# Kernel tuning notes

Measured on AMD Instinct MI355X. Metric: run time of the kernel, lower is better.

Reference implementation:

```python
import jax, jax.numpy as jnp
import numpy as np

N, M, KNN, KUP, POS_DIM = 15872, 35637, 5, 20, 32


def _pos_emb_table(n, d):
    # transformer-style sinusoidal table (matches PosEmb._define_pos_emb)
    pos = np.arange(n, dtype=np.float32)[:, None]
    i2 = np.arange(0, d, 2, dtype=np.float32)
    div = 10000.0 ** (i2 / d)
    pe = np.zeros((n, d), dtype=np.float32)
    pe[:, 0::2] = np.sin(pos / div)
    pe[:, 1::2] = np.cos(pos / div)
    return jnp.asarray(pe)


def _lrelu(x):
    return jnp.where(x > 0, x, 0.2 * x)


def _gather(x, idx):
    # x: [B,n,d], idx: [B,m,k] -> [B,m,k,d]
    return jax.vmap(lambda xb, ib: xb[ib])(x, idx)


def _knn_idx(x, k):
    # x: [B,n,d]; k nearest excluding self (torch knn drops column 0 of topk)
    xx = jnp.sum(x * x, axis=-1)
    neg = 2.0 * jnp.einsum('bnd,bmd->bnm', x, x) - xx[:, :, None] - xx[:, None, :]
    _, idx = jax.lax.top_k(neg, k + 1)
    return idx[..., 1:]


def _emb_block(feat, idx, ec_w1, ec_s1, ec_h1, ec_w2, ec_b2,
               w1, s1, h1, w2, s2, h2, w3, s3, h3, w4, b4):
    # get_graph_feature: [B,n,k,2*in] = cat(nbr - ctr, ctr)
    nbr = _gather(feat, idx)
    ctr = jnp.broadcast_to(feat[:, :, None, :], nbr.shape)
    e = jnp.concatenate([nbr - ctr, ctr], axis=-1)
    # edge_conv (1x1 conv2d = per-edge linear); BN folded into scale/shift (eval mode)
    e = _lrelu(jnp.einsum('bnkc,oc->bnko', e, ec_w1) * ec_s1 + ec_h1)
    e = jnp.einsum('bnkc,oc->bnko', e, ec_w2) + ec_b2
    f1 = jnp.max(e, axis=2)                                   # max over k neighbors -> [B,n,out]
    fmax = jnp.broadcast_to(jnp.max(f1, axis=1, keepdims=True), f1.shape)
    favg = jnp.broadcast_to(jnp.mean(f1, axis=1, keepdims=True), f1.shape)
    h = jnp.concatenate([feat, f1, fmax, favg], axis=-1)      # [B,n,3*out+in]
    # fc_out: 1x1 conv1d stack = per-point MLP with folded BN + LeakyReLU
    h = _lrelu(h @ w1.T * s1 + h1)
    h = _lrelu(h @ w2.T * s2 + h2)
    h = _lrelu(h @ w3.T * s3 + h3)
    return h @ w4.T + b4


def _forward(lx, ldx, pos_emb,
             b0_ec_w1, b0_ec_s1, b0_ec_h1, b0_ec_w2, b0_ec_b2,
             b0_fc_w1, b0_fc_s1, b0_fc_h1, b0_fc_w2, b0_fc_s2, b0_fc_h2,
             b0_fc_w3, b0_fc_s3, b0_fc_h3, b0_fc_w4, b0_fc_b4,
             b1_ec_w1, b1_ec_s1, b1_ec_h1, b1_ec_w2, b1_ec_b2,
             b1_fc_w1, b1_fc_s1, b1_fc_h1, b1_fc_w2, b1_fc_s2, b1_fc_h2,
             b1_fc_w3, b1_fc_s3, b1_fc_h3, b1_fc_w4, b1_fc_b4,
             up_inputs, up_w0, up_s0, up_h0, up_w_rest, up_s_rest, up_h_rest, up_wf, up_bf,
             dec_w0, dec_b0, dec_w1, dec_b1, dec_w2, dec_b2, dec_w3, dec_b3,
             dec_w4, dec_b4, dec_wf, dec_bf,
             idx0, up_idx):
    B = ldx.shape[0]
    feat_in = jnp.concatenate([ldx, jnp.broadcast_to(pos_emb[None], (B,) + pos_emb.shape)], axis=-1)  # [B,N,35]
    f0 = _emb_block(feat_in, idx0,
                    b0_ec_w1, b0_ec_s1, b0_ec_h1, b0_ec_w2, b0_ec_b2,
                    b0_fc_w1, b0_fc_s1, b0_fc_h1, b0_fc_w2, b0_fc_s2, b0_fc_h2,
                    b0_fc_w3, b0_fc_s3, b0_fc_h3, b0_fc_w4, b0_fc_b4)   # [B,N,64]
    idx1 = _knn_idx(f0, KNN)                                            # dynamic feature-space KNN
    f1 = _emb_block(f0, idx1,
                    b1_ec_w1, b1_ec_s1, b1_ec_h1, b1_ec_w2, b1_ec_b2,
                    b1_fc_w1, b1_fc_s1, b1_fc_h1, b1_fc_w2, b1_fc_s2, b1_fc_h2,
                    b1_fc_w3, b1_fc_s3, b1_fc_h3, b1_fc_w4, b1_fc_b4)   # [B,N,128]
    x_feat = jnp.concatenate([feat_in, f0, f1], axis=-1)                # [B,N,227]
    # Upscale: SIREN-activated 1x1-conv stack -> softmax interpolation weights over KUP lo-res nbrs
    h = jnp.sin(jnp.einsum('bmkc,oc->bmko', up_inputs[:B], up_w0) * up_s0 + up_h0)
    for i in range(up_w_rest.shape[0]):
        h = jnp.sin(jnp.einsum('bmkc,oc->bmko', h, up_w_rest[i]) * up_s_rest[i] + up_h_rest[i])
    logits = jnp.einsum('bmkc,oc->bmko', h, up_wf) + up_bf              # [B,M,KUP,1]
    w = jax.nn.softmax(logits, axis=2)
    grouped = _gather(x_feat, up_idx)                                   # [B,M,KUP,227]
    z = jnp.sum(w * grouped, axis=2)                                    # [B,M,227]
    # SIREN decoder: dims [227,256,128,64,32,16,3]; zip with 5 mods applies first 5 layers + head
    h = jnp.sin(30.0 * (z @ dec_w0.T + dec_b0))
    h = jnp.sin(h @ dec_w1.T + dec_b1)
    h = jnp.sin(h @ dec_w2.T + dec_b2)
    h = jnp.sin(h @ dec_w3.T + dec_b3)
    h = jnp.sin(h @ dec_w4.T + dec_b4)
    return h @ dec_wf.T + dec_bf                                        # [B,M,3]


def setup_inputs():
    key = jax.random.key(0)
    ks = iter(jax.random.split(key, 100))
    def rn(*s):
        return jax.random.normal(next(ks), s, jnp.float32) * 0.05
    def sc(*s):
        return jax.random.uniform(next(ks), s, jnp.float32, minval=0.5, maxval=1.5)
    inp = {}
    inp['lx'] = jax.random.normal(next(ks), (1, N, 3), jnp.float32)
    inp['ldx'] = jax.random.normal(next(ks), (1, N, 3), jnp.float32)
    inp['pos_emb'] = _pos_emb_table(N, POS_DIM)
    inp['idx0'] = jax.random.randint(next(ks), (1, N, KNN), 0, N - 1)
    # EmbModule 0: in=35, out=64
    inp['b0_ec_w1'], inp['b0_ec_s1'], inp['b0_ec_h1'] = rn(128, 70), sc(128), rn(128)
    inp['b0_ec_w2'], inp['b0_ec_b2'] = rn(64, 128), rn(64)
    inp['b0_fc_w1'], inp['b0_fc_s1'], inp['b0_fc_h1'] = rn(192, 227), sc(192), rn(192)
    inp['b0_fc_w2'], inp['b0_fc_s2'], inp['b0_fc_h2'] = rn(128, 192), sc(128), rn(128)
    inp['b0_fc_w3'], inp['b0_fc_s3'], inp['b0_fc_h3'] = rn(64, 128), sc(64), rn(64)
    inp['b0_fc_w4'], inp['b0_fc_b4'] = rn(64, 64), rn(64)
    # EmbModule 1: in=64, out=128
    inp['b1_ec_w1'], inp['b1_ec_s1'], inp['b1_ec_h1'] = rn(256, 128), sc(256), rn(256)
    inp['b1_ec_w2'], inp['b1_ec_b2'] = rn(128, 256), rn(128)
    inp['b1_fc_w1'], inp['b1_fc_s1'], inp['b1_fc_h1'] = rn(384, 448), sc(384), rn(384)
    inp['b1_fc_w2'], inp['b1_fc_s2'], inp['b1_fc_h2'] = rn(256, 384), sc(256), rn(256)
    inp['b1_fc_w3'], inp['b1_fc_s3'], inp['b1_fc_h3'] = rn(128, 256), sc(128), rn(128)
    inp['b1_fc_w4'], inp['b1_fc_b4'] = rn(128, 128), rn(128)
    inp['up_inputs'] = jax.random.uniform(next(ks), (1, M, KUP, 7), jnp.float32)
    inp['up_idx'] = jax.random.randint(next(ks), (1, M, KUP), 0, N - 1)
    inp['up_w0'], inp['up_s0'], inp['up_h0'] = rn(128, 7), sc(128), rn(128)
    inp['up_w_rest'], inp['up_s_rest'], inp['up_h_rest'] = rn(7, 128, 128), sc(7, 128), rn(7, 128)
    inp['up_wf'], inp['up_bf'] = rn(1, 128), rn(1)
    # SIREN decoder
    dd = [227, 256, 128, 64, 32, 16]
    for i in range(5):
        inp['dec_w%d' % i], inp['dec_b%d' % i] = rn(dd[i + 1], dd[i]), rn(dd[i + 1])
    inp['dec_wf'], inp['dec_bf'] = rn(3, 16), rn(3)
    return inp


def reference(lx, ldx, pos_emb, idx0,
              b0_ec_w1, b0_ec_s1, b0_ec_h1, b0_ec_w2, b0_ec_b2,
              b0_fc_w1, b0_fc_s1, b0_fc_h1, b0_fc_w2, b0_fc_s2, b0_fc_h2,
              b0_fc_w3, b0_fc_s3, b0_fc_h3, b0_fc_w4, b0_fc_b4,
              b1_ec_w1, b1_ec_s1, b1_ec_h1, b1_ec_w2, b1_ec_b2,
              b1_fc_w1, b1_fc_s1, b1_fc_h1, b1_fc_w2, b1_fc_s2, b1_fc_h2,
              b1_fc_w3, b1_fc_s3, b1_fc_h3, b1_fc_w4, b1_fc_b4,
              up_inputs, up_idx, up_w0, up_s0, up_h0,
              up_w_rest, up_s_rest, up_h_rest, up_wf, up_bf,
              dec_w0, dec_b0, dec_w1, dec_b1, dec_w2, dec_b2, dec_w3, dec_b3,
              dec_w4, dec_b4, dec_wf, dec_bf):
    return _forward(lx, ldx, pos_emb,
                    b0_ec_w1, b0_ec_s1, b0_ec_h1, b0_ec_w2, b0_ec_b2,
                    b0_fc_w1, b0_fc_s1, b0_fc_h1, b0_fc_w2, b0_fc_s2, b0_fc_h2,
                    b0_fc_w3, b0_fc_s3, b0_fc_h3, b0_fc_w4, b0_fc_b4,
                    b1_ec_w1, b1_ec_s1, b1_ec_h1, b1_ec_w2, b1_ec_b2,
                    b1_fc_w1, b1_fc_s1, b1_fc_h1, b1_fc_w2, b1_fc_s2, b1_fc_h2,
                    b1_fc_w3, b1_fc_s3, b1_fc_h3, b1_fc_w4, b1_fc_b4,
                    up_inputs, up_w0, up_s0, up_h0, up_w_rest, up_s_rest, up_h_rest, up_wf, up_bf,
                    dec_w0, dec_b0, dec_w1, dec_b1, dec_w2, dec_b2, dec_w3, dec_b3,
                    dec_w4, dec_b4, dec_wf, dec_bf,
                    idx0, up_idx)
```

## Files before the change

### kernel.cpp

```cpp
#include <hip/hip_runtime.h>
#include <hip/hip_bf16.h>
#include <math.h>

#define N_PTS 15872
#define M_PTS 35637
#define KNN_K 5
#define KUP   20
#define UP_ROWS (M_PTS * KUP)
#define NTILE (N_PTS/32)
#define N_EDGE (N_PTS*KNN_K)
#define CDIV(a,b) (((a)+(b)-1)/(b))

typedef __hip_bfloat16 bf16;
typedef unsigned int uint;
typedef unsigned short ushort_t;
__device__ __forceinline__ float b2f(bf16 x){ return __bfloat162float(x); }

__device__ __forceinline__ uint f2bf_bits(float x){
  uint u = __float_as_uint(x);
  return (u + 0x7FFFu + ((u>>16)&1u)) >> 16;
}

__device__ __forceinline__ ushort_t f2h_bits(float x){
  union { _Float16 h; ushort_t u; } c; c.h = (_Float16)x; return c.u;
}

typedef __attribute__((ext_vector_type(8))) short bf16x8;
typedef __attribute__((ext_vector_type(8))) _Float16 f16x8;
typedef __attribute__((ext_vector_type(2))) __fp16 fp16x2_t;
typedef __attribute__((ext_vector_type(16))) float f32x16;
union FragAB { bf16x8 v; uint u[4]; };
union FragB  { bf16x8 v; uint4 q; };
union FragH  { f16x8 v; uint4 q; _Float16 h[8]; };
union Acc16  { f32x16 v; float f[16]; };
union H2U    { fp16x2_t h; uint u; };

__global__ void flag_k(const uint* __restrict__ pos_raw, int* __restrict__ flag){
  if (threadIdx.x == 0 && blockIdx.x == 0)
    flag[0] = (pos_raw[0] == 0x3F800000u) ? 1 : 0;
}

struct CvtTab { const void* src[52]; int start[52]; };
__global__ __launch_bounds__(256) void cvt_all_k(CvtTab tab, float* __restrict__ dst,
                                                 const int* __restrict__ flag, int total){
  int i = blockIdx.x*256 + threadIdx.x;
  if (i >= total) return;
  int s = 0;
#pragma unroll 1
  for (int k = 1; k < 52; k++) if (tab.start[k] <= i) s = k;
  int off = i - tab.start[s];
  float v = flag[0] ? b2f(((const bf16*)tab.src[s])[off]) : ((const float*)tab.src[s])[off];
  dst[i] = v;
}

__global__ void packfrag16_k(const float* __restrict__ w, const float* __restrict__ sr,
                             ushort_t* __restrict__ out, int n){
  int i = blockIdx.x*256 + threadIdx.x;
  if (i >= n) return;
  int j = i & 7;
  int lam = (i >> 3) & 63;
  int fg = i >> 9;
  int t = fg & 3, ks = (fg >> 2) & 1, Q = (fg >> 3) & 3, l = fg >> 5;
  int nn = t*32 + (lam & 31);
  int kk = Q*32 + ks*16 + ((j>>2)<<3) + ((lam>>5)<<2) + (j&3);
  float x = w[l*16384 + nn*128 + kk] * sr[l*128 + nn];
  out[i] = f2h_bits(x);
}

struct PackTab { const float* src[18]; int N[18], K[18], ldk[18], Kpad[18], start[18]; };
__global__ __launch_bounds__(256) void packw_all_k(PackTab t, ushort_t* __restrict__ whi,
                                                   ushort_t* __restrict__ wlo, int total){
  int i = blockIdx.x*256 + threadIdx.x;
  if (i >= total) return;
  int s = 0;
#pragma unroll 1
  for (int q = 1; q < 18; q++) if (t.start[q] <= i) s = q;
  int ii = i - t.start[s];
  int j = ii & 7;
  int lane = (ii >> 3) & 63;
  int fr = ii >> 9;
  int nq = t.Kpad[s] >> 5;
  int ks = fr & 1;
  int q  = (fr >> 1) % nq;
  int nt = (fr >> 1) / nq;
  int n = nt*32 + (lane & 31);
  int k = q*32 + ks*16 + (lane >> 5)*8 + j;
  float x = (n < t.N[s] && k < t.K[s]) ? t.src[s][(size_t)n*t.ldk[s] + k] : 0.f;
  uint hb = f2bf_bits(x);
  uint lb = f2bf_bits(x - __uint_as_float(hb << 16));
  whi[i] = (ushort_t)hb;
  wlo[i] = (ushort_t)lb;
}

__global__ void packknn_k(const float* __restrict__ xf, const float* __restrict__ nr,
                          ushort_t* __restrict__ ahi, ushort_t* __restrict__ alo,
                          ushort_t* __restrict__ bhi, ushort_t* __restrict__ blo){
  int i = blockIdx.x*256 + threadIdx.x;
  if (i >= NTILE*5*64*8) return;
  int e = i & 7;
  int lane = (i >> 3) & 63;
  int rest = i >> 9;
  int kc = rest % 5, jt = rest / 5;
  int n = jt*32 + (lane & 31);
  int k = kc*16 + (lane >> 5)*8 + e;
  float f = (k < 64) ? xf[(size_t)n*227 + 35 + k] : 0.f;
  float av, bv;
  if (k < 64)      { av = 2.f*f;   bv = f; }
  else if (k == 64){ av = nr[n];   bv = -1.f; }
  else if (k == 65){ av = 1.f;     bv = -nr[n]; }
  else             { av = 0.f;     bv = 0.f; }
  uint ah = f2bf_bits(av); uint al = f2bf_bits(av - __uint_as_float(ah<<16));
  uint bh = f2bf_bits(bv); uint bl = f2bf_bits(bv - __uint_as_float(bh<<16));
  ahi[i] = (ushort_t)ah; alo[i] = (ushort_t)al;
  bhi[i] = (ushort_t)bh; blo[i] = (ushort_t)bl;
}

__global__ void fillmark_k(bf16* __restrict__ out, int n){
  int i = blockIdx.x*256 + threadIdx.x;
  if (i < n) out[i] = __float2bfloat16(12345.0f);
}

template<int ACT>
__global__ __launch_bounds__(256) void gemm_mfma_k(
    const float* __restrict__ A, int lda, int K, int M,
    const ushort_t* __restrict__ wh, const ushort_t* __restrict__ wl,
    int woff, int KqTot,
    const float* __restrict__ scale, const float* __restrict__ shift,
    float* __restrict__ C, int ldc, int N)
{
  __shared__ __align__(16) uint slab[64*128];
  const int tid = threadIdx.x;
  const int lane = tid & 63;
  const int wv = tid >> 6;
  const int np = lane & 31;
  const int hb2 = lane >> 5;
  const int rhalf = wv & 1, thalf = wv >> 1;
  const int rb = blockIdx.x * 64;
  const int tbase = blockIdx.y * 4;
  const int row_l = rhalf*32 + np;
  int NtLoc = (N >> 5) - tbase; if (NtLoc > 4) NtLoc = 4;

  Acc16 acc[2];
#pragma unroll
  for (int u=0;u<2;u++)
#pragma unroll
    for (int i=0;i<16;i++) acc[u].f[i] = 0.f;

#pragma unroll 1
  for (int k0 = 0; k0 < K; k0 += 128) {
    for (int e = tid; e < 64*32; e += 256) {
      int r = e >> 5, g = e & 31;
      int gr = rb + r;
      uint p[4];
#pragma unroll
      for (int u=0;u<4;u++){
        int k = k0 + g*4 + u;
        float f = (gr < M && k < K) ? A[(size_t)gr*lda + k] : 0.f;
        uint hb = f2bf_bits(f);
        uint lb = f2bf_bits(f - __uint_as_float(hb<<16));
        p[u] = (hb<<16) | lb;
      }
      *(uint4*)&slab[r*128 + (((g ^ r) & 31)<<2)] = make_uint4(p[0],p[1],p[2],p[3]);
    }
    __syncthreads();
    int qb = k0 >> 5;
    int KqLoc = KqTot - qb; if (KqLoc > 4) KqLoc = 4;
#pragma unroll 1
    for (int q = 0; q < KqLoc; q++){
#pragma unroll
      for (int ks = 0; ks < 2; ks++){
        int g0 = q*8 + ks*4 + hb2*2;
        uint4 a0 = *(const uint4*)&slab[row_l*128 + ((((g0  ) ^ row_l) & 31)<<2)];
        uint4 a1 = *(const uint4*)&slab[row_l*128 + ((((g0+1) ^ row_l) & 31)<<2)];
        uint au[8] = {a0.x,a0.y,a0.z,a0.w,a1.x,a1.y,a1.z,a1.w};
        FragAB ah, al;
#pragma unroll
        for (int p=0;p<4;p++){
          ah.u[p] = (au[2*p]>>16)     | (au[2*p+1] & 0xFFFF0000u);
          al.u[p] = (au[2*p]&0xFFFFu) | (au[2*p+1]<<16);
        }
#pragma unroll
        for (int u=0;u<2;u++){
          int t = thalf + u*2;
          if (t < NtLoc){
            size_t fb = (size_t)woff + ((size_t)(((tbase+t)*KqTot + qb + q)*2 + ks))*512 + (size_t)lane*8;
            FragB bh, bl;
            bh.q = *(const uint4*)(wh + fb);
            bl.q = *(const uint4*)(wl + fb);
            acc[u].v = __builtin_amdgcn_mfma_f32_32x32x16_bf16(ah.v, bh.v, acc[u].v, 0,0,0);
            acc[u].v = __builtin_amdgcn_mfma_f32_32x32x16_bf16(al.v, bh.v, acc[u].v, 0,0,0);
            acc[u].v = __builtin_amdgcn_mfma_f32_32x32x16_bf16(ah.v, bl.v, acc[u].v, 0,0,0);
          }
        }
      }
    }
    __syncthreads();
  }

#pragma unroll
  for (int u=0;u<2;u++){
    int t = thalf + u*2;
    if (t < NtLoc){
      int col = (tbase+t)*32 + np;
      float scv = scale[col], shv = shift[col];
#pragma unroll
      for (int reg=0;reg<16;reg++){
        int r32 = (reg&3) + 8*(reg>>2) + 4*hb2;
        int gr = rb + rhalf*32 + r32;
        if (gr < M){
          float v = acc[u].f[reg]*scv + shv;
          if (ACT==1) v = v > 0.f ? v : 0.2f*v;
          C[(size_t)gr*ldc + col] = v;
        }
      }
    }
  }
}

struct MLayer { int K, N, Kq, Nt, woff, soff, hoff, epi, act; float gmul; };
struct MCfg { MLayer L[6]; };

template<int NL, int OUTMODE>
__global__ __launch_bounds__(256) void mlp_fused_k(
    const float* __restrict__ A0, int lda0, int K0, int M,
    MCfg cfg,
    const ushort_t* __restrict__ wh, const ushort_t* __restrict__ wl,
    const float* __restrict__ wc,
    float* __restrict__ Cout, int ldc,
    void* __restrict__ oflg, const int* __restrict__ flag)
{
  __shared__ __align__(16) uint slab[64*256];
  const int tid = threadIdx.x;
  const int lane = tid & 63;
  const int wv = tid >> 6;
  const int np = lane & 31;
  const int hb2 = lane >> 5;
  const int rhalf = wv & 1, thalf = wv >> 1;
  const int rb = blockIdx.x * 64;
  const int row_l = rhalf*32 + np;

  for (int e = tid; e < 64*64; e += 256) {
    int r = e >> 6, g = e & 63;
    int gr = rb + r;
    uint p[4];
#pragma unroll
    for (int u=0;u<4;u++){
      int k = g*4+u;
      float f = (gr < M && k < K0) ? A0[(size_t)gr*lda0 + k] : 0.f;
      uint hb = f2bf_bits(f);
      uint lb = f2bf_bits(f - __uint_as_float(hb<<16));
      p[u] = (hb<<16) | lb;
    }
    *(uint4*)&slab[r*256 + (((g ^ r) & 63)<<2)] = make_uint4(p[0],p[1],p[2],p[3]);
  }
  __syncthreads();

#pragma unroll 1
  for (int l = 0; l < NL; l++){
    const int N = cfg.L[l].N, Kq = cfg.L[l].Kq, Nt = cfg.L[l].Nt;
    const int woff = cfg.L[l].woff, soff = cfg.L[l].soff, hoff = cfg.L[l].hoff;
    const int epi = cfg.L[l].epi, actf = cfg.L[l].act;
    const float gmul = cfg.L[l].gmul;
    Acc16 acc[4];
#pragma unroll
    for (int u=0;u<4;u++)
#pragma unroll
      for (int i=0;i<16;i++) acc[u].f[i] = 0.f;

#pragma unroll 1
    for (int q = 0; q < Kq; q++){
#pragma unroll
      for (int ks = 0; ks < 2; ks++){
        int g0 = (q*32 + ks*16 + hb2*8) >> 2;
        uint4 a0 = *(const uint4*)&slab[row_l*256 + ((((g0  ) ^ row_l) & 63)<<2)];
        uint4 a1 = *(const uint4*)&slab[row_l*256 + ((((g0+1) ^ row_l) & 63)<<2)];
        uint au[8] = {a0.x,a0.y,a0.z,a0.w,a1.x,a1.y,a1.z,a1.w};
        FragAB ah, al;
#pragma unroll
        for (int p=0;p<4;p++){
          ah.u[p] = (au[2*p]>>16)     | (au[2*p+1] & 0xFFFF0000u);
          al.u[p] = (au[2*p]&0xFFFFu) | (au[2*p+1]<<16);
        }
#pragma unroll
        for (int u=0;u<4;u++){
          int t = thalf + u*2;
          if (t < Nt){
            size_t fb = (size_t)woff + ((size_t)((t*Kq + q)*2 + ks))*512 + (size_t)lane*8;
            FragB bh, bl;
            bh.q = *(const uint4*)(wh + fb);
            bl.q = *(const uint4*)(wl + fb);
            acc[u].v = __builtin_amdgcn_mfma_f32_32x32x16_bf16(ah.v, bh.v, acc[u].v, 0,0,0);
            acc[u].v = __builtin_amdgcn_mfma_f32_32x32x16_bf16(al.v, bh.v, acc[u].v, 0,0,0);
            acc[u].v = __builtin_amdgcn_mfma_f32_32x32x16_bf16(ah.v, bl.v, acc[u].v, 0,0,0);
          }
        }
      }
    }
    __syncthreads();
#pragma unroll
    for (int u=0;u<4;u++){
      int t = thalf + u*2;
      if (t < Nt){
        int col = t*32 + np;
        if (col < N){
          float scv = (epi==0) ? wc[soff+col] : 0.f;
          float shv = wc[hoff+col];
#pragma unroll
          for (int reg=0;reg<16;reg++){
            int r32 = (reg&3) + 8*(reg>>2) + 4*hb2;
            float v = acc[u].f[reg];
            if (epi==0)      v = v*scv + shv;
            else if (epi==1) v = v + shv;
            else             v = (v + shv)*gmul;
            if (actf==1)      v = v > 0.f ? v : 0.2f*v;
            else if (actf==2) v = __sinf(v);
            if (l == NL-1){
              int gr = rb + rhalf*32 + r32;
              if (gr < M){
                if (OUTMODE==0) Cout[(size_t)gr*ldc + col] = v;
                else {
                  if (!(fabsf(v) < 1e30f)) v = 777.0f;
                  size_t oi = (size_t)gr*3 + col;
                  if (flag[0]) ((bf16*)oflg)[oi] = __float2bfloat16(v);
                  else         ((float*)oflg)[oi] = v;
                }
              }
            } else {
              int r = rhalf*32 + r32;
              uint hb = f2bf_bits(v);
              uint lb = f2bf_bits(v - __uint_as_float(hb<<16));
              slab[r*256 + ((((col>>2) ^ r) & 63)<<2) + (col&3)] = (hb<<16) | lb;
            }
          }
        }
      }
    }
    __syncthreads();
  }
}

#define INS5(tv, tj, v, j) \
  if ((v) > tv[4]){ tv[4]=(v); tj[4]=(j); \
    _Pragma("unroll") \
    for (int q=4;q>0;q--) \
      if (tv[q] > tv[q-1]){ float tf=tv[q-1]; tv[q-1]=tv[q]; tv[q]=tf; \
                            int ti=tj[q-1]; tj[q-1]=tj[q]; tj[q]=ti; } }

__global__ __launch_bounds__(256) void knn_mfma_k(
    const ushort_t* __restrict__ ahi, const ushort_t* __restrict__ alo,
    const ushort_t* __restrict__ bhi, const ushort_t* __restrict__ blo,
    int* __restrict__ out)
{
  __shared__ float mv[4][32][5];
  __shared__ int   mjj[4][32][5];
  const int tid = threadIdx.x;
  const int lane = tid & 63;
  const int wv = tid >> 6;
  const int np = lane & 31;
  const int hb2 = lane >> 5;
  const int it = blockIdx.x;
  const int ig = it*32 + np;

  FragB vh[5], vl[5];
  {
    size_t bb = (size_t)(it*5)*512 + (size_t)lane*8;
#pragma unroll
    for (int kc=0;kc<5;kc++){
      vh[kc].q = *(const uint4*)(bhi + bb + kc*512);
      vl[kc].q = *(const uint4*)(blo + bb + kc*512);
    }
  }

  float tv[5] = {-1e30f,-1e30f,-1e30f,-1e30f,-1e30f};
  int   tj[5] = {0,0,0,0,0};

  FragB uh[5], ul[5], nh[5], nl[5];
  {
    size_t ab = (size_t)(wv*5)*512 + (size_t)lane*8;
#pragma unroll
    for (int kc=0;kc<5;kc++){
      uh[kc].q = *(const uint4*)(ahi + ab + kc*512);
      ul[kc].q = *(const uint4*)(alo + ab + kc*512);
    }
  }

#pragma unroll 1
  for (int t = 0; t < NTILE/4; t++){
    int jt = wv + t*4;
    if (t+1 < NTILE/4){
      size_t an = (size_t)((jt+4)*5)*512 + (size_t)lane*8;
#pragma unroll
      for (int kc=0;kc<5;kc++){
        nh[kc].q = *(const uint4*)(ahi + an + kc*512);
        nl[kc].q = *(const uint4*)(alo + an + kc*512);
      }
    }
    Acc16 acc;
#pragma unroll
    for (int q=0;q<16;q++) acc.f[q] = 0.f;
#pragma unroll
    for (int kc=0;kc<5;kc++){
      acc.v = __builtin_amdgcn_mfma_f32_32x32x16_bf16(uh[kc].v, vh[kc].v, acc.v, 0,0,0);
      acc.v = __builtin_amdgcn_mfma_f32_32x32x16_bf16(ul[kc].v, vh[kc].v, acc.v, 0,0,0);
      acc.v = __builtin_amdgcn_mfma_f32_32x32x16_bf16(uh[kc].v, vl[kc].v, acc.v, 0,0,0);
    }
    int jb = jt*32 + 4*hb2;
#pragma unroll
    for (int reg=0;reg<16;reg++){
      int j = jb + (reg&3) + 8*(reg>>2);
      float v = acc.f[reg];
      if (j != ig) { INS5(tv, tj, v, j); }
    }
    if (t+1 < NTILE/4){
#pragma unroll
      for (int kc=0;kc<5;kc++){ uh[kc] = nh[kc]; ul[kc] = nl[kc]; }
    }
  }

#pragma unroll
  for (int s=0;s<5;s++){
    float ov = __shfl_xor(tv[s], 32, 64);
    int   oj = __shfl_xor(tj[s], 32, 64);
    INS5(tv, tj, ov, oj);
  }
  if (hb2 == 0){
#pragma unroll
    for (int s=0;s<5;s++){ mv[wv][np][s] = tv[s]; mjj[wv][np][s] = tj[s]; }
  }
  __syncthreads();
  if (tid < 32){
    float bv[5]; int bj[5];
#pragma unroll
    for (int s=0;s<5;s++){ bv[s] = mv[0][tid][s]; bj[s] = mjj[0][tid][s]; }
#pragma unroll
    for (int w=1;w<4;w++)
#pragma unroll
      for (int s=0;s<5;s++){
        float v = mv[w][tid][s]; int j = mjj[w][tid][s];
        INS5(bv, bj, v, j);
      }
    int gi = it*32 + tid;
#pragma unroll
    for (int s=0;s<5;s++) out[gi*KNN_K + s] = bj[s];
  }
}

__global__ __launch_bounds__(256) void siren_fused_k(
    const void* __restrict__ upin,
    const ushort_t* __restrict__ wf16,
    const float* __restrict__ W0c, const float* __restrict__ S0c, const float* __restrict__ H0c,
    const float* __restrict__ HRc,
    const float* __restrict__ WFc, const float* __restrict__ BFc,
    float* __restrict__ logits, const int* __restrict__ flag)
{
  __shared__ float intile[4*32*8];
  __shared__ __align__(16) float w0s[128*8];
  __shared__ __align__(16) float hrs[7*128];
  __shared__ __align__(16) float wfs[128];
  __shared__ float bfs[1];

  const int tid  = threadIdx.x;
  const int lane = tid & 63;
  const int wv   = tid >> 6;
  const int np   = lane & 31;
  const int hb2  = lane >> 5;
  const int rowbase = blockIdx.x * 128 + wv * 32;
  const int isbf = flag[0];
  float* intw = intile + wv*32*8;

  for (int e = tid; e < 128*7; e += 256){
    int c = e/7, k = e%7;
    w0s[c*8+k] = W0c[e]*S0c[c];
  }
  if (tid < 128) w0s[tid*8+7] = H0c[tid];
  for (int e = tid; e < 7*128; e += 256) hrs[e] = HRc[e];
  if (tid < 128) wfs[tid] = WFc[tid];
  if (tid == 0) bfs[0] = BFc[0];
  for (int e = lane; e < 32*7; e += 64) {
    int r = e/7, k = e%7;
    int gr = rowbase + r;
    float v = 0.f;
    if (gr < UP_ROWS)
      v = isbf ? b2f(((const bf16*)upin)[(size_t)gr*7+k]) : ((const float*)upin)[(size_t)gr*7+k];
    intw[r*8+k] = v;
  }
  __syncthreads();

  uint st0[16], st1[16];
  {
    float xin[7];
#pragma unroll
    for (int k=0;k<7;k++) xin[k] = intw[np*8+k];
#pragma unroll
    for (int g = 0; g < 16; g++){
      float xs[4];
#pragma unroll
      for (int j = 0; j < 4; j++){
        int c = g*8 + hb2*4 + j;
        const float4 wa = *(const float4*)&w0s[c*8];
        const float4 wb = *(const float4*)&w0s[c*8+4];
        float a = wb.w;
        a += xin[0]*wa.x; a += xin[1]*wa.y; a += xin[2]*wa.z; a += xin[3]*wa.w;
        a += xin[4]*wb.x; a += xin[5]*wb.y; a += xin[6]*wb.z;
        xs[j] = __sinf(a);
      }
      H2U u0,u1;
      u0.h = __builtin_amdgcn_cvt_pkrtz(xs[0],xs[1]);
      u1.h = __builtin_amdgcn_cvt_pkrtz(xs[2],xs[3]);
      st0[g] = u0.u; st1[g] = u1.u;
    }
  }

  FragH fr[8];
#pragma unroll
  for (int m = 0; m < 8; m++)
    fr[m].q = make_uint4(st0[2*m], st1[2*m], st0[2*m+1], st1[2*m+1]);

  uint nst0[16], nst1[16];
#pragma unroll 1
  for (int l = 0; l < 7; l++) {
#pragma unroll
    for (int tp = 0; tp < 2; tp++){
      Acc16 acc0, acc1;
#pragma unroll
      for (int i=0;i<16;i++){ acc0.f[i] = 0.f; acc1.f[i] = 0.f; }
#pragma unroll
      for (int m = 0; m < 8; m++){
        int fb = (((l*8 + m)*4 + tp*2) << 9) + lane*8;
        FragH bh0, bh1;
        bh0.q = *(const uint4*)(wf16 + fb);
        bh1.q = *(const uint4*)(wf16 + fb + 512);
        acc0.v = __builtin_amdgcn_mfma_f32_32x32x16_f16(bh0.v, fr[m].v, acc0.v, 0,0,0);
        acc1.v = __builtin_amdgcn_mfma_f32_32x32x16_f16(bh1.v, fr[m].v, acc1.v, 0,0,0);
      }
#pragma unroll
      for (int rg = 0; rg < 4; rg++){
        int g0 = (tp*2+0)*4 + rg;
        const float4 b0v = *(const float4*)&hrs[l*128 + g0*8 + hb2*4];
        float x0 = __sinf(acc0.f[rg*4+0] + b0v.x);
        float x1 = __sinf(acc0.f[rg*4+1] + b0v.y);
        float x2 = __sinf(acc0.f[rg*4+2] + b0v.z);
        float x3 = __sinf(acc0.f[rg*4+3] + b0v.w);
        H2U u0,u1;
        u0.h = __builtin_amdgcn_cvt_pkrtz(x0,x1);
        u1.h = __builtin_amdgcn_cvt_pkrtz(x2,x3);
        nst0[g0] = u0.u; nst1[g0] = u1.u;

        int g1 = (tp*2+1)*4 + rg;
        const float4 b1v = *(const float4*)&hrs[l*128 + g1*8 + hb2*4];
        float y0 = __sinf(acc1.f[rg*4+0] + b1v.x);
        float y1 = __sinf(acc1.f[rg*4+1] + b1v.y);
        float y2 = __sinf(acc1.f[rg*4+2] + b1v.z);
        float y3 = __sinf(acc1.f[rg*4+3] + b1v.w);
        H2U v0,v1;
        v0.h = __builtin_amdgcn_cvt_pkrtz(y0,y1);
        v1.h = __builtin_amdgcn_cvt_pkrtz(y2,y3);
        nst0[g1] = v0.u; nst1[g1] = v1.u;
      }
    }
    if (l < 6){
#pragma unroll
      for (int m = 0; m < 8; m++)
        fr[m].q = make_uint4(nst0[2*m], nst1[2*m], nst0[2*m+1], nst1[2*m+1]);
    }
  }

  {
    float a = 0.f;
#pragma unroll
    for (int g = 0; g < 16; g++){
      const float4 w4 = *(const float4*)&wfs[g*8 + hb2*4];
      H2U u0,u1; u0.u = nst0[g]; u1.u = nst1[g];
      a += (float)u0.h.x*w4.x + (float)u0.h.y*w4.y
         + (float)u1.h.x*w4.z + (float)u1.h.y*w4.w;
    }
    a += __shfl_xor(a, 32, 64);
    int gr = rowbase + np;
    if (hb2 == 0 && gr < UP_ROWS) logits[gr] = a + bfs[0];
  }
}

__global__ void featin_k(const void* __restrict__ ldx, const void* __restrict__ pos,
                         float* __restrict__ xf, const int* __restrict__ flag){
  int i = blockIdx.x*256 + threadIdx.x;
  if (i >= N_PTS*35) return;
  int n = i / 35, c = i % 35;
  float v;
  if (flag[0]) {
    v = (c < 3) ? b2f(((const bf16*)ldx)[n*3+c]) : b2f(((const bf16*)pos)[n*32 + (c-3)]);
  } else {
    v = (c < 3) ? ((const float*)ldx)[n*3+c] : ((const float*)pos)[n*32 + (c-3)];
  }
  xf[(size_t)n*227 + c] = v;
}

__global__ void gather_e_k(const float* __restrict__ xf, int coff, int CIN,
                           const int* __restrict__ idx, float* __restrict__ e,
                           int n0, int np){
  int W2 = 2*CIN;
  int i = blockIdx.x*256 + threadIdx.x;
  if (i >= np*KNN_K*W2) return;
  int c = i % W2; int ek = i / W2;
  int nl = ek / KNN_K, k = ek % KNN_K;
  int n = n0 + nl;
  int j = idx[n*KNN_K + k];
  float out;
  if (c < CIN) out = xf[(size_t)j*227 + coff + c] - xf[(size_t)n*227 + coff + c];
  else         out = xf[(size_t)n*227 + coff + (c-CIN)];
  e[(size_t)ek*W2 + c] = out;
}

__global__ void kmax_k(const float* __restrict__ e2, int C, int ld, float* __restrict__ f1,
                       int n0, int np){
  int i = blockIdx.x*256 + threadIdx.x;
  if (i >= np*C) return;
  int nl = i / C, c = i % C;
  float v = -1e30f;
  for (int k=0;k<KNN_K;k++) v = fmaxf(v, e2[((size_t)nl*KNN_K+k)*ld + c]);
  f1[(size_t)(n0+nl)*C + c] = v;
}

template<int C>
__global__ __launch_bounds__(256) void reduce1_k(const float* __restrict__ X, int n,
                                                 float* __restrict__ pmax, float* __restrict__ psum){
  const int tid = threadIdx.x;
  const int c = tid % C;
  const int r0 = tid / C;
  const int TPR = 256 / C;
  float vmax = -1e30f, vsum = 0.f;
  for (int row = blockIdx.x * TPR + r0; row < n; row += gridDim.x * TPR) {
    float v = X[(size_t)row * C + c];
    vmax = fmaxf(vmax, v); vsum += v;
  }
  __shared__ float smax[256], ssum[256];
  smax[tid]=vmax; ssum[tid]=vsum;
  __syncthreads();
  if (tid < C) {
    for (int q=1;q<TPR;q++){ vmax=fmaxf(vmax, smax[q*C+c]); vsum += ssum[q*C+c]; }
    pmax[blockIdx.x*C + c] = vmax; psum[blockIdx.x*C + c] = vsum;
  }
}

template<int C>
__global__ __launch_bounds__(256) void red2fold_k(
    const float* __restrict__ pmax, const float* __restrict__ psum,
    int nblk, float invn,
    const float* __restrict__ W, int ldw, int off1, int off2,
    const float* __restrict__ scale, const float* __restrict__ shift,
    float* __restrict__ out, int N)
{
  __shared__ float smax[C], ssum[C];
  int tid = threadIdx.x;
  if (tid < C){
    float vmax=-1e30f, vsum=0.f;
    for (int b=0;b<nblk;b++){ vmax=fmaxf(vmax,pmax[b*C+tid]); vsum+=psum[b*C+tid]; }
    smax[tid]=vmax; ssum[tid]=vsum*invn;
  }
  __syncthreads();
  for (int n = tid; n < N; n += 256){
    const float* wr = W + (size_t)n*ldw;
    float s = 0.f;
    for (int j=0;j<C;j++) s += wr[off1+j]*smax[j];
    for (int j=0;j<C;j++) s += wr[off2+j]*ssum[j];
    out[n] = s*scale[n] + shift[n];
  }
}

__global__ void concat2_k(const float* __restrict__ xf, int coff, int CF,
                          const float* __restrict__ f1, int C,
                          float* __restrict__ h, int n0, int np){
  int W = CF + C;
  int i = blockIdx.x*256 + threadIdx.x;
  if (i >= np*W) return;
  int nl = i / W, c = i % W;
  int n = n0 + nl;
  float v = (c < CF) ? xf[(size_t)n*227 + coff + c] : f1[(size_t)n*C + (c-CF)];
  h[(size_t)nl*W + c] = v;
}

__global__ void norms_k(const float* __restrict__ xf, float* __restrict__ nr){
  int n = blockIdx.x*256 + threadIdx.x;
  if (n >= N_PTS) return;
  const float* p = xf + (size_t)n*227 + 35;
  float s = 0.f;
  for (int d=0;d<64;d++) s += p[d]*p[d];
  nr[n] = s;
}

__global__ __launch_bounds__(256) void softgather_k(const float* __restrict__ logits,
                                                    const int* __restrict__ up_idx,
                                                    const float* __restrict__ xf,
                                                    float* __restrict__ z){
  __shared__ float lw[4][KUP]; __shared__ int li[4][KUP];
  int sub = threadIdx.x >> 6;
  int tid = threadIdx.x & 63;
  int m = blockIdx.x*4 + sub;
  bool ok = (m < M_PTS);
  if (ok && tid < KUP){
    lw[sub][tid] = logits[(size_t)m*KUP + tid];
    li[sub][tid] = up_idx[(size_t)m*KUP + tid];
  }
  __syncthreads();
  if (ok){
    float mx = -1e30f;
    for (int k=0;k<KUP;k++) mx = fmaxf(mx, lw[sub][k]);
    float w[KUP]; float s = 0.f;
    for (int k=0;k<KUP;k++){ w[k] = expf(lw[sub][k]-mx); s += w[k]; }
    float inv = 1.f/s;
    for (int c = tid; c < 227; c += 64){
      float acc = 0.f;
      for (int k=0;k<KUP;k++) acc += w[k] * xf[(size_t)li[sub][k]*227 + c];
      z[(size_t)m*227 + c] = acc*inv;
    }
  }
}

extern "C" void kernel_launch(void* const* d_in, const int* in_sizes, int n_in,
                              void* d_out, int out_size, void* d_ws, size_t ws_size,
                              hipStream_t stream) {
  const int *idx0  = (const int*)d_in[3];
  const int *upidx = (const int*)d_in[37];

  float* ws = (float*)d_ws;
  float* x_feat = ws;
  float* f1b    = ws + 3602944;
  float* pmax   = ws + 5634560;
  float* psum   = ws + 5667328;
  float* fold0  = pmax + 24576;
  float* fold1  = psum + 24576;
  int*   flag   = (int*)(ws + 5700352);
  int*   idx1   = (int*)(ws + 5700368);
  float* nrm    = ws + 5779728;
  float* logits = ws + 5795600;
  float* wcvt   = ws + 6508352;
  float* S      = ws + 7214400;
  ushort_t* whi  = (ushort_t*)(S + 9662464);
  ushort_t* wlo  = whi + 114688;
  ushort_t* gwhi = wlo + 114688;
  ushort_t* gwlo = gwhi + 503808;

  const size_t NEED = (size_t)(7214400 + 9662464) * 4
                    + (size_t)(114688*2 + 503808*2) * 2;
  if (ws_size < NEED) {
    fillmark_k<<<CDIV(out_size,256),256,0,stream>>>((bf16*)d_out, out_size);
    return;
  }

  flag_k<<<1,64,0,stream>>>((const uint*)d_in[2], flag);
  CvtTab tab;
  int wcoff = 0, seg = 0;
  auto CVT = [&](int i, int n)->const float* {
    tab.src[seg] = d_in[i]; tab.start[seg] = wcoff; seg++;
    const float* p = wcvt + wcoff; wcoff += n;
    return p;
  };
  const float *E0W1=CVT(4,8960),  *E0S1=CVT(5,128),  *E0H1=CVT(6,128),
              *E0W2=CVT(7,8192),  *E0B2=CVT(8,64);
  const float *F0W1=CVT(9,43584), *F0S1=CVT(10,192), *F0H1=CVT(11,192),
              *F0W2=CVT(12,24576),*F0S2=CVT(13,128), *F0H2=CVT(14,128),
              *F0W3=CVT(15,8192), *F0S3=CVT(16,64),  *F0H3=CVT(17,64),
              *F0W4=CVT(18,4096), *F0B4=CVT(19,64);
  const float *E1W1=CVT(20,32768),*E1S1=CVT(21,256), *E1H1=CVT(22,256),
              *E1W2=CVT(23,32768),*E1B2=CVT(24,128);
  const float *F1W1=CVT(25,172032),*F1S1=CVT(26,384),*F1H1=CVT(27,384),
              *F1W2=CVT(28,98304),*F1S2=CVT(29,256), *F1H2=CVT(30,256),
              *F1W3=CVT(31,32768),*F1S3=CVT(32,128), *F1H3=CVT(33,128),
              *F1W4=CVT(34,16384),*F1B4=CVT(35,128);
  const float *UPW0=CVT(38,896),  *UPS0=CVT(39,128), *UPH0=CVT(40,128),
              *UPWR=CVT(41,114688),*UPSR=CVT(42,896),*UPHR=CVT(43,896),
              *UPWF=CVT(44,128),  *UPBF=CVT(45,1);
  const float *DW0=CVT(46,58112), *DB0=CVT(47,256),
              *DW1=CVT(48,32768), *DB1=CVT(49,128),
              *DW2=CVT(50,8192),  *DB2=CVT(51,64),
              *DW3=CVT(52,2048),  *DB3=CVT(53,32),
              *DW4=CVT(54,512),   *DB4=CVT(55,16),
              *DWF=CVT(56,48),    *DBF=CVT(57,3);
  cvt_all_k<<<CDIV(wcoff,256),256,0,stream>>>(tab, wcvt, flag, wcoff);

  packfrag16_k<<<CDIV(114688,256),256,0,stream>>>(UPWR, UPSR, whi, 114688);

  PackTab ptab;
  int offs[18];
  int ptotal = 0;
  {
    int q = 0;
    auto REG = [&](const float* s, int N, int K, int ldk, int Kpad){
      ptab.src[q]=s; ptab.N[q]=N; ptab.K[q]=K; ptab.ldk[q]=ldk; ptab.Kpad[q]=Kpad;
      ptab.start[q]=ptotal; offs[q]=ptotal;
      ptotal += CDIV(N,32)*32*Kpad; q++;
    };
    REG(F0W1,192, 99,227,128);
    REG(F0W2,128,192,192,192); REG(F0W3,64,128,128,128); REG(F0W4,64,64,64,64);
    REG(DW0,256,227,227,256);  REG(DW1,128,256,256,256);  REG(DW2,64,128,128,128);
    REG(DW3,32,64,64,64);      REG(DW4,16,32,32,32);      REG(DWF,3,16,16,32);
    REG(E0W1,128,70,70,96);    REG(E0W2,64,128,128,128);
    REG(E1W1,256,128,128,128); REG(E1W2,128,256,256,256);
    REG(F1W3,128,256,256,256); REG(F1W4,128,128,128,128);
    REG(F1W1,384,192,448,192);
    REG(F1W2,256,384,384,384);
  }
  packw_all_k<<<CDIV(ptotal,256),256,0,stream>>>(ptab, gwhi, gwlo, ptotal);

  auto OFF = [&](const float* p){ return (int)(p - wcvt); };
  const int HOFF0 = (int)(fold0 - wcvt);
  MCfg cfc0{};
  cfc0.L[0] = { 99,192,4,6, offs[0], OFF(F0S1), HOFF0,     0,1, 0.f};
  cfc0.L[1] = {192,128,6,4, offs[1], OFF(F0S2), OFF(F0H2), 0,1, 0.f};
  cfc0.L[2] = {128, 64,4,2, offs[2], OFF(F0S3), OFF(F0H3), 0,1, 0.f};
  cfc0.L[3] = { 64, 64,2,2, offs[3], 0,         OFF(F0B4), 1,0, 0.f};
  MCfg cdec{};
  cdec.L[0] = {227,256,8,8, offs[4], 0, OFF(DB0), 2,2, 30.f};
  cdec.L[1] = {256,128,8,4, offs[5], 0, OFF(DB1), 1,2, 0.f};
  cdec.L[2] = {128, 64,4,2, offs[6], 0, OFF(DB2), 1,2, 0.f};
  cdec.L[3] = { 64, 32,2,1, offs[7], 0, OFF(DB3), 1,2, 0.f};
  cdec.L[4] = { 32, 16,1,1, offs[8], 0, OFF(DB4), 1,2, 0.f};
  cdec.L[5] = { 16,  3,1,1, offs[9], 0, OFF(DBF), 1,0, 0.f};
  MCfg ce0{};
  ce0.L[0] = { 70,128,3,4, offs[10], OFF(E0S1), OFF(E0H1), 0,1, 0.f};
  ce0.L[1] = {128, 64,4,2, offs[11], 0,         OFF(E0B2), 1,0, 0.f};
  MCfg ce1{};
  ce1.L[0] = {128,256,4,8, offs[12], OFF(E1S1), OFF(E1H1), 0,1, 0.f};
  ce1.L[1] = {256,128,8,4, offs[13], 0,         OFF(E1B2), 1,0, 0.f};
  MCfg cf1t{};
  cf1t.L[0] = {256,128,8,4, offs[14], OFF(F1S3), OFF(F1H3), 0,1, 0.f};
  cf1t.L[1] = {128,128,4,4, offs[15], 0,         OFF(F1B4), 1,0, 0.f};

  const float invN = 1.f/(float)N_PTS;

  featin_k<<<CDIV(N_PTS*35,256),256,0,stream>>>(d_in[1], d_in[2], x_feat, flag);

  {
    float* eA = S;
    gather_e_k<<<CDIV(N_EDGE*70,256),256,0,stream>>>(x_feat, 0, 35, idx0, eA, 0, N_PTS);
    mlp_fused_k<2,0><<<CDIV(N_EDGE,64),256,0,stream>>>(
        eA,70,70,N_EDGE, ce0, gwhi,gwlo,wcvt, eA,70, nullptr, flag);
    kmax_k<<<CDIV(N_PTS*64,256),256,0,stream>>>(eA, 64, 70, f1b, 0, N_PTS);
  }
  reduce1_k<64><<<256,256,0,stream>>>(f1b, N_PTS, pmax, psum);
  red2fold_k<64><<<1,256,0,stream>>>(pmax, psum, 256, invN,
                                     F0W1,227, 99,163, F0S1,F0H1, fold0, 192);
  {
    float* h = S;
    concat2_k<<<CDIV(N_PTS*99,256),256,0,stream>>>(x_feat,0,35, f1b,64, h, 0, N_PTS);
    mlp_fused_k<4,0><<<CDIV(N_PTS,64),256,0,stream>>>(
        h,99,99,N_PTS, cfc0, gwhi,gwlo,wcvt, x_feat+35,227, nullptr, flag);
  }

  norms_k<<<CDIV(N_PTS,256),256,0,stream>>>(x_feat, nrm);
  {
    const int PLANE = NTILE*5*64*8;
    ushort_t* ajhi = (ushort_t*)S;
    ushort_t* ajlo = ajhi + PLANE;
    ushort_t* bihi = ajlo + PLANE;
    ushort_t* bilo = bihi + PLANE;
    packknn_k<<<CDIV(PLANE,256),256,0,stream>>>(x_feat, nrm, ajhi, ajlo, bihi, bilo);
    knn_mfma_k<<<NTILE,256,0,stream>>>(ajhi, ajlo, bihi, bilo, idx1);
  }

  {
    const int P1 = 7936;
    for (int n0 = 0; n0 < N_PTS; n0 += P1) {
      int np = N_PTS - n0; if (np > P1) np = P1;
      int ne = np * KNN_K;
      float* eA = S;
      gather_e_k<<<CDIV(ne*128,256),256,0,stream>>>(x_feat, 35, 64, idx1, eA, n0, np);
      mlp_fused_k<2,0><<<CDIV(ne,64),256,0,stream>>>(
          eA,128,128,ne, ce1, gwhi,gwlo,wcvt, eA,128, nullptr, flag);
      kmax_k<<<CDIV(np*128,256),256,0,stream>>>(eA, 128, 128, f1b, n0, np);
    }
  }
  reduce1_k<128><<<256,256,0,stream>>>(f1b, N_PTS, pmax, psum);
  red2fold_k<128><<<1,256,0,stream>>>(pmax, psum, 256, invN,
                                      F1W1,448, 192,320, F1S1,F1H1, fold1, 384);
  {
    float* h  = S;
    float* a1 = S + 3047424;
    int gx = CDIV(N_PTS,64);
    concat2_k<<<CDIV(N_PTS*192,256),256,0,stream>>>(x_feat,35,64, f1b,128, h, 0, N_PTS);
    gemm_mfma_k<1><<<dim3(gx,3),256,0,stream>>>(h,192,192,N_PTS, gwhi,gwlo, offs[16],6,
                                                F1S1,fold1, a1,384, 384);
    gemm_mfma_k<1><<<dim3(gx,2),256,0,stream>>>(a1,384,384,N_PTS, gwhi,gwlo, offs[17],12,
                                                F1S2,F1H2, h,256, 256);
    mlp_fused_k<2,0><<<gx,256,0,stream>>>(
        h,256,256,N_PTS, cf1t, gwhi,gwlo,wcvt, x_feat+99,227, nullptr, flag);
  }

  siren_fused_k<<<CDIV(UP_ROWS,128),256,0,stream>>>(
      d_in[36], whi, UPW0, UPS0, UPH0, UPHR, UPWF, UPBF, logits, flag);
  float* zbuf = S;
  softgather_k<<<CDIV(M_PTS,4),256,0,stream>>>(logits, upidx, x_feat, zbuf);

  mlp_fused_k<6,1><<<CDIV(M_PTS,64),256,0,stream>>>(
      zbuf,227,227,M_PTS, cdec, gwhi,gwlo,wcvt, nullptr,0, d_out, flag);
}
```

Measured before the change: 1.772 ms.

## Prescale SIREN weights by 1/2pi, use native sin, stage layer weights in LDS

The SIREN kernel's weights, first-layer bias and hidden biases are now prescaled by 1/(2π), so the hardware sine builtin, which takes its argument in revolutions, can be called directly without a multiply. Hidden-layer biases are loaded into the MFMA accumulators up front instead of being added after the matrix product. Each layer's fp16 weight fragments are copied cooperatively into 32 KB of LDS, with barriers around each use, rather than every wave reading them from global memory. The extra LDS and two barriers per layer may lower occupancy and add stalls, and the prescaling shifts fp16 rounding of the weights slightly.

```diff
diff --git a/kernel.cpp b/kernel.cpp
--- a/kernel.cpp
+++ b/kernel.cpp
@@ -10,6 +10,7 @@
 #define NTILE (N_PTS/32)
 #define N_EDGE (N_PTS*KNN_K)
 #define CDIV(a,b) (((a)+(b)-1)/(b))
+#define INV2PI 0.15915494309189535f
 
 typedef __hip_bfloat16 bf16;
 typedef unsigned int uint;
@@ -23,6 +24,14 @@
 
 __device__ __forceinline__ ushort_t f2h_bits(float x){
   union { _Float16 h; ushort_t u; } c; c.h = (_Float16)x; return c.u;
+}
+
+__device__ __forceinline__ float sinrev(float x){
+#if __has_builtin(__builtin_amdgcn_sinf)
+  return __builtin_amdgcn_sinf(x);
+#else
+  return __sinf(x * 6.283185307179586f);
+#endif
 }
 
 typedef __attribute__((ext_vector_type(8))) short bf16x8;
@@ -63,7 +72,7 @@
   int t = fg & 3, ks = (fg >> 2) & 1, Q = (fg >> 3) & 3, l = fg >> 5;
   int nn = t*32 + (lam & 31);
   int kk = Q*32 + ks*16 + ((j>>2)<<3) + ((lam>>5)<<2) + (j&3);
-  float x = w[l*16384 + nn*128 + kk] * sr[l*128 + nn];
+  float x = w[l*16384 + nn*128 + kk] * sr[l*128 + nn] * INV2PI;
   out[i] = f2h_bits(x);
 }
 
@@ -453,6 +462,7 @@
     const float* __restrict__ WFc, const float* __restrict__ BFc,
     float* __restrict__ logits, const int* __restrict__ flag)
 {
+  __shared__ __align__(16) ushort_t wlds[16384];
   __shared__ float intile[4*32*8];
   __shared__ __align__(16) float w0s[128*8];
   __shared__ __align__(16) float hrs[7*128];
@@ -470,10 +480,10 @@
 
   for (int e = tid; e < 128*7; e += 256){
     int c = e/7, k = e%7;
-    w0s[c*8+k] = W0c[e]*S0c[c];
-  }
-  if (tid < 128) w0s[tid*8+7] = H0c[tid];
-  for (int e = tid; e < 7*128; e += 256) hrs[e] = HRc[e];
+    w0s[c*8+k] = W0c[e]*S0c[c]*INV2PI;
+  }
+  if (tid < 128) w0s[tid*8+7] = H0c[tid]*INV2PI;
+  for (int e = tid; e < 7*128; e += 256) hrs[e] = HRc[e]*INV2PI;
   if (tid < 128) wfs[tid] = WFc[tid];
   if (tid == 0) bfs[0] = BFc[0];
   for (int e = lane; e < 32*7; e += 64) {
@@ -502,7 +512,7 @@
         float a = wb.w;
         a += xin[0]*wa.x; a += xin[1]*wa.y; a += xin[2]*wa.z; a += xin[3]*wa.w;
         a += xin[4]*wb.x; a += xin[5]*wb.y; a += xin[6]*wb.z;
-        xs[j] = __sinf(a);
+        xs[j] = sinrev(a);
       }
       H2U u0,u1;
       u0.h = __builtin_amdgcn_cvt_pkrtz(xs[0],xs[1]);
@@ -519,45 +529,56 @@
   uint nst0[16], nst1[16];
 #pragma unroll 1
   for (int l = 0; l < 7; l++) {
+    {
+      const uint4* src = (const uint4*)(wf16 + l*16384);
+      uint4* dst = (uint4*)wlds;
+#pragma unroll
+      for (int e = 0; e < 8; e++) dst[tid + e*256] = src[tid + e*256];
+    }
+    __syncthreads();
 #pragma unroll
     for (int tp = 0; tp < 2; tp++){
       Acc16 acc0, acc1;
 #pragma unroll
-      for (int i=0;i<16;i++){ acc0.f[i] = 0.f; acc1.f[i] = 0.f; }
+      for (int rg = 0; rg < 4; rg++){
+        const float4 b0 = *(const float4*)&hrs[l*128 + ((tp*2+0)*4+rg)*8 + hb2*4];
+        acc0.f[rg*4+0]=b0.x; acc0.f[rg*4+1]=b0.y; acc0.f[rg*4+2]=b0.z; acc0.f[rg*4+3]=b0.w;
+        const float4 b1 = *(const float4*)&hrs[l*128 + ((tp*2+1)*4+rg)*8 + hb2*4];
+        acc1.f[rg*4+0]=b1.x; acc1.f[rg*4+1]=b1.y; acc1.f[rg*4+2]=b1.z; acc1.f[rg*4+3]=b1.w;
+      }
 #pragma unroll
       for (int m = 0; m < 8; m++){
-        int fb = (((l*8 + m)*4 + tp*2) << 9) + lane*8;
+        int fb = ((m*4 + tp*2) << 9) + lane*8;
         FragH bh0, bh1;
-        bh0.q = *(const uint4*)(wf16 + fb);
-        bh1.q = *(const uint4*)(wf16 + fb + 512);
+        bh0.q = *(const uint4*)&wlds[fb];
+        bh1.q = *(const uint4*)&wlds[fb + 512];
         acc0.v = __builtin_amdgcn_mfma_f32_32x32x16_f16(bh0.v, fr[m].v, acc0.v, 0,0,0);
         acc1.v = __builtin_amdgcn_mfma_f32_32x32x16_f16(bh1.v, fr[m].v, acc1.v, 0,0,0);
       }
 #pragma unroll
       for (int rg = 0; rg < 4; rg++){
         int g0 = (tp*2+0)*4 + rg;
-        const float4 b0v = *(const float4*)&hrs[l*128 + g0*8 + hb2*4];
-        float x0 = __sinf(acc0.f[rg*4+0] + b0v.x);
-        float x1 = __sinf(acc0.f[rg*4+1] + b0v.y);
-        float x2 = __sinf(acc0.f[rg*4+2] + b0v.z);
-        float x3 = __sinf(acc0.f[rg*4+3] + b0v.w);
+        float x0 = sinrev(acc0.f[rg*4+0]);
+        float x1 = sinrev(acc0.f[rg*4+1]);
+        float x2 = sinrev(acc0.f[rg*4+2]);
+        float x3 = sinrev(acc0.f[rg*4+3]);
         H2U u0,u1;
         u0.h = __builtin_amdgcn_cvt_pkrtz(x0,x1);
         u1.h = __builtin_amdgcn_cvt_pkrtz(x2,x3);
         nst0[g0] = u0.u; nst1[g0] = u1.u;
 
         int g1 = (tp*2+1)*4 + rg;
-        const float4 b1v = *(const float4*)&hrs[l*128 + g1*8 + hb2*4];
-        float y0 = __sinf(acc1.f[rg*4+0] + b1v.x);
-        float y1 = __sinf(acc1.f[rg*4+1] + b1v.y);
-        float y2 = __sinf(acc1.f[rg*4+2] + b1v.z);
-        float y3 = __sinf(acc1.f[rg*4+3] + b1v.w);
+        float y0 = sinrev(acc1.f[rg*4+0]);
+        float y1 = sinrev(acc1.f[rg*4+1]);
+        float y2 = sinrev(acc1.f[rg*4+2]);
+        float y3 = sinrev(acc1.f[rg*4+3]);
         H2U v0,v1;
         v0.h = __builtin_amdgcn_cvt_pkrtz(y0,y1);
         v1.h = __builtin_amdgcn_cvt_pkrtz(y2,y3);
         nst0[g1] = v0.u; nst1[g1] = v1.u;
       }
     }
+    __syncthreads();
     if (l < 6){
 #pragma unroll
       for (int m = 0; m < 8; m++)
```

New measurement: 1.889 ms. 6.6% more time.
